# Performance work log

Measured on AMD Instinct MI355X. Metric: run time of the kernel, lower is better.

The kernel has to match this reference:

```python
import jax, jax.numpy as jnp
import numpy as np
import math

NUM_CONVS = 4
GN_GROUPS = 32
GN_EPS = 1e-5
FPN_STRIDES = (8, 16, 32, 64, 128)
PRIOR_PROB = 0.01


def conv3x3(x, w, b):
    # x: [N,C,H,W], w: [O,I,3,3]
    y = jax.lax.conv_general_dilated(
        x, w, window_strides=(1, 1), padding='SAME',
        dimension_numbers=('NCHW', 'OIHW', 'NCHW'))
    return y + b[None, :, None, None]


def group_norm(x, gamma, beta):
    n, c, h, w = x.shape
    xg = x.reshape(n, GN_GROUPS, c // GN_GROUPS, h, w)
    mean = xg.mean(axis=(2, 3, 4), keepdims=True)
    var = xg.var(axis=(2, 3, 4), keepdims=True)
    xn = ((xg - mean) * jax.lax.rsqrt(var + GN_EPS)).reshape(n, c, h, w)
    return xn * gamma[None, :, None, None] + beta[None, :, None, None]


def subnet(x, ws, bs, gws, gbs):
    # NUM_CONVS x (conv3x3 -> GN -> ReLU)
    for i in range(NUM_CONVS):
        x = jax.nn.relu(group_norm(conv3x3(x, ws[i], bs[i]), gws[i], gbs[i]))
    return x


def permute_to_N_HWA_K(x, k):
    n = x.shape[0]
    return x.transpose(0, 2, 3, 1).reshape(n, -1, k)


def setup_inputs() -> dict:
    key = jax.random.key(0)
    ks = jax.random.split(key, 16)
    C, K = 256, 80
    feats = {
        'p3': jax.random.normal(ks[0], (1, C, 80, 80), jnp.float32),
        'p4': jax.random.normal(ks[1], (1, C, 40, 40), jnp.float32),
        'p5': jax.random.normal(ks[2], (1, C, 20, 20), jnp.float32),
        'p6': jax.random.normal(ks[3], (1, C, 10, 10), jnp.float32),
        'p7': jax.random.normal(ks[4], (1, C, 5, 5), jnp.float32),
    }
    std = 0.01
    bias_value = -math.log((1 - PRIOR_PROB) / PRIOR_PROB)
    params = {
        'cls_w': std * jax.random.normal(ks[5], (NUM_CONVS, C, C, 3, 3), jnp.float32),
        'cls_b': jnp.zeros((NUM_CONVS, C), jnp.float32),
        'cls_gn_w': jnp.ones((NUM_CONVS, C), jnp.float32),
        'cls_gn_b': jnp.zeros((NUM_CONVS, C), jnp.float32),
        'box_w': std * jax.random.normal(ks[6], (NUM_CONVS, C, C, 3, 3), jnp.float32),
        'box_b': jnp.zeros((NUM_CONVS, C), jnp.float32),
        'box_gn_w': jnp.ones((NUM_CONVS, C), jnp.float32),
        'box_gn_b': jnp.zeros((NUM_CONVS, C), jnp.float32),
        'score_w': std * jax.random.normal(ks[7], (K, C, 3, 3), jnp.float32),
        'score_b': jnp.full((K,), bias_value, jnp.float32),
        'pred_w': std * jax.random.normal(ks[8], (4, C, 3, 3), jnp.float32),
        'pred_b': jnp.zeros((4,), jnp.float32),
        'iou_w': std * jax.random.normal(ks[9], (1, C, 3, 3), jnp.float32),
        'iou_b': jnp.zeros((1,), jnp.float32),
        'scales': jnp.ones((5,), jnp.float32),
    }
    return {**feats, **params}


def reference(p3, p4, p5, p6, p7,
              cls_w, cls_b, cls_gn_w, cls_gn_b,
              box_w, box_b, box_gn_w, box_gn_b,
              score_w, score_b, pred_w, pred_b, iou_w, iou_b, scales):
    features = [p3, p4, p5, p6, p7]
    logits, bbox_reg, ious = [], [], []
    for l, feat in enumerate(features):
        c = subnet(feat, cls_w, cls_b, cls_gn_w, cls_gn_b)
        b = subnet(feat, box_w, box_b, box_gn_w, box_gn_b)
        logit = conv3x3(c, score_w, score_b)          # [N,80,H,W]
        iou = conv3x3(b, iou_w, iou_b)                # [N,1,H,W]
        bp = conv3x3(b, pred_w, pred_b) * scales[l]   # Scale module
        # norm_reg_targets=True branch
        reg = jax.nn.relu(bp) * FPN_STRIDES[l]        # [N,4,H,W]
        logits.append(permute_to_N_HWA_K(logit, 80))
        bbox_reg.append(permute_to_N_HWA_K(reg, 4))
        ious.append(permute_to_N_HWA_K(iou, 1))
    box_cls = jnp.concatenate(logits, axis=1)    # [N, sumHW, 80]
    box_delta = jnp.concatenate(bbox_reg, axis=1)  # [N, sumHW, 4]
    box_iou = jnp.concatenate(ious, axis=1)      # [N, sumHW, 1]
    # pack into one array for a single output: [N, sumHW, 85]
    return jnp.concatenate([box_cls, box_delta, box_iou], axis=-1)
```

## Files before the change

### kernel.cpp

```cpp
#include <hip/hip_runtime.h>

typedef unsigned short u16;
typedef __attribute__((ext_vector_type(8))) short bf16x8;
typedef __attribute__((ext_vector_type(4))) float f32x4;

#define NLEV 5
#define CCH 256
#define KTOT 2304
#define P_TOT 8525
#define PP_TOT 9165
#define PLS (PP_TOT*64)
#define HSTR 11776

__constant__ int   c_HW[NLEV]     = {6400, 1600, 400, 100, 25};
__constant__ int   c_W[NLEV]      = {80, 40, 20, 10, 5};
__constant__ int   c_off[NLEV]    = {0, 6400, 8000, 8400, 8500};
__constant__ int   c_poff[NLEV]   = {0, 6724, 8488, 8972, 9116};
__constant__ int   c_tls[NLEV+1]  = {0, 50, 65, 71, 73, 74};
__constant__ int   c_ntx[NLEV]    = {5, 3, 2, 1, 1};
__constant__ float c_stridef[NLEV]= {8.f, 16.f, 32.f, 64.f, 128.f};

__device__ __forceinline__ u16 f2bf(float f){
  union { float f; unsigned u; } v; v.f = f;
  unsigned r = v.u + 0x7fffu + ((v.u >> 16) & 1u);
  return (u16)(r >> 16);
}

__device__ __forceinline__ void g2l16(const u16* g, u16* l, int lane){
#if defined(__has_builtin)
#if __has_builtin(__builtin_amdgcn_global_load_lds)
  __builtin_amdgcn_global_load_lds(
      (const __attribute__((address_space(1))) unsigned int*)g,
      (__attribute__((address_space(3))) unsigned int*)l, 16, 0, 0);
  return;
#endif
#endif
  *(uint4*)(l + lane*8) = *(const uint4*)g;
}

#define WAIT_VM12  0x0F7C

template<int MODE>
__global__ __launch_bounds__(128, 2) void gemm_conv(
    const u16* __restrict__ Xc, const u16* __restrict__ Xb,
    const u16* __restrict__ Wc, const u16* __restrict__ Wb,
    const float* __restrict__ bc, const float* __restrict__ bb,
    float* __restrict__ Yc, float* __restrict__ Yb,
    float* __restrict__ stats,
    const float* __restrict__ predb, const float* __restrict__ ioub,
    const float* __restrict__ scales, float* __restrict__ out)
{
  __shared__ u16 hB[2*HSTR];
  __shared__ float sstat[8][2];

  const int ptile = blockIdx.x;
  const int mtile = blockIdx.y;
  const int br = blockIdx.z;
  int lv = 0;
  #pragma unroll
  for (int i = 1; i < NLEV; i++) if (ptile >= c_tls[i]) lv = i;
  const int tidx = ptile - c_tls[lv];
  const int ntx = c_ntx[lv];
  const int ty0 = (tidx / ntx) * 8, tx0 = (tidx - (tidx / ntx) * ntx) * 16;
  const int W = c_W[lv], wrow2 = W + 2;

  const int tid = threadIdx.x, wv = tid >> 6, ln = tid & 63;
  const int quad = ln >> 4, l15 = ln & 15;

  const u16* __restrict__ X  = br ? Xb : Xc;
  const u16* __restrict__ WA = br ? Wb : Wc;

  const int SZ = (MODE == 0) ? 16384 : 8192;
  const int g2 = mtile*2 + wv;
  const u16* aln = WA + (size_t)(g2*2048 + ln*8);

  const u16* hptr[12]; int hslab[12];
  #pragma unroll
  for (int i = 0; i < 12; i++) {
    int j = wv + 2*i;
    if (j > 22) j -= 2;
    hslab[i] = j;
    const int item = j*64 + ln;
    int hp = item >> 3; if (hp >= 180) hp -= 180;
    const int g = item & 7;
    const int hy = hp / 18, hx = hp - hy*18;
    const int prow = c_poff[lv] + (ty0 + hy)*wrow2 + tx0 + hx;
    hptr[i] = X + (size_t)prow*64 + ((g ^ (hp & 7)) << 3);
  }

  auto stageH = [&](int plane) {
    u16* dst = &hB[(plane & 1) * HSTR];
    const size_t cof = (size_t)plane * PLS;
    #pragma unroll
    for (int i = 0; i < 12; i++)
      g2l16(hptr[i] + cof, dst + hslab[i]*512, ln);
  };

  f32x4 acc[2][8];
  #pragma unroll
  for (int i = 0; i < 2; i++)
    #pragma unroll
    for (int j = 0; j < 8; j++) acc[i][j] = (f32x4){0.f, 0.f, 0.f, 0.f};

  bf16x8 af[3][2][2];
  auto loadA = [&](int cc_, int dw_) {
    #pragma unroll
    for (int dh = 0; dh < 3; dh++) {
      const u16* p = aln + (size_t)((dh*3 + dw_)*4 + cc_) * SZ;
      #pragma unroll
      for (int sub = 0; sub < 2; sub++)
        #pragma unroll
        for (int mt = 0; mt < 2; mt++)
          af[dh][sub][mt] = *(const bf16x8*)(p + (sub*2 + mt)*512);
    }
  };

  if (MODE == 0 && tid < 16) sstat[tid >> 1][tid & 1] = 0.f;

  stageH(0);
  stageH(1);
  loadA(0, 0);
  __syncthreads();

  int cc = 0, dw = 0;
  #pragma unroll 1
  for (int u = 0; u < 12; u++) {
    if (dw == 0 && cc > 0) {
      __builtin_amdgcn_s_waitcnt(WAIT_VM12);
      __builtin_amdgcn_sched_barrier(0);
      __builtin_amdgcn_s_barrier();
      __builtin_amdgcn_sched_barrier(0);
      if (cc < 3) stageH(cc + 1);
    }
    const u16* hpl = &hB[(cc & 1) * HSTR];
    #pragma unroll
    for (int sub = 0; sub < 2; sub++) {
      const int q = sub*4 + quad;
      bf16x8 bf[10];
      #pragma unroll
      for (int n2 = 0; n2 < 10; n2++) {
        const int hp = n2*18 + l15 + dw;
        bf[n2] = *(const bf16x8*)&hpl[hp*64 + ((q ^ (hp & 7)) << 3)];
      }
      #pragma unroll
      for (int dh = 0; dh < 3; dh++)
        #pragma unroll
        for (int mt = 0; mt < 2; mt++)
          #pragma unroll
          for (int nt = 0; nt < 8; nt++)
            acc[mt][nt] = __builtin_amdgcn_mfma_f32_16x16x32_bf16(
                af[dh][sub][mt], bf[nt + dh], acc[mt][nt], 0, 0, 0);
    }
    int dwn = dw + 1, ccn = cc;
    if (dwn == 3) { dwn = 0; ccn++; }
    if (u < 11) loadA(ccn, dwn);
    dw = dwn; cc = ccn;
  }

  const int gx = tx0 + l15;
  if (MODE == 0) {
    const float* __restrict__ bias = br ? bb : bc;
    float* __restrict__ Y = br ? Yb : Yc;
    #pragma unroll
    for (int mt = 0; mt < 2; mt++) {
      const int mloc = wv*32 + mt*16 + quad*4;
      const int mrow = mtile*64 + mloc;
      const f32x4 bv = *(const f32x4*)&bias[mrow];
      float s = 0.f, sq = 0.f;
      #pragma unroll
      for (int nt = 0; nt < 8; nt++) {
        const int gy = ty0 + nt;
        f32x4 v = acc[mt][nt] + bv;
        if (gy < W && gx < W) {
          const size_t n = (size_t)(c_off[lv] + gy*W + gx);
          *(f32x4*)&Y[n*CCH + mrow] = v;
          #pragma unroll
          for (int r = 0; r < 4; r++) { s += v[r]; sq += v[r]*v[r]; }
        }
      }
      #pragma unroll
      for (int o = 1; o < 16; o <<= 1) { s += __shfl_xor(s, o); sq += __shfl_xor(sq, o); }
      if (l15 == 0) {
        const int g = mloc >> 3;
        atomicAdd(&sstat[g][0], s);
        atomicAdd(&sstat[g][1], sq);
      }
    }
    __syncthreads();
    if (tid < 16) {
      const int g = tid >> 1, c = tid & 1;
      atomicAdd(&stats[((br*NLEV + lv)*32 + mtile*8 + g)*2 + c], sstat[g][c]);
    }
  } else {
    const float scl = scales[lv];
    const float stf = c_stridef[lv];
    #pragma unroll
    for (int mt = 0; mt < 2; mt++) {
      const int mr0 = mtile*64 + wv*32 + mt*16 + quad*4;
      if (mr0 >= 85) continue;
      #pragma unroll
      for (int nt = 0; nt < 8; nt++) {
        const int gy = ty0 + nt;
        if (gy >= W || gx >= W) continue;
        const size_t n = (size_t)(c_off[lv] + gy*W + gx);
        const f32x4 v = acc[mt][nt];
        #pragma unroll
        for (int r = 0; r < 4; r++) {
          const int m = mr0 + r;
          if (br == 0) {
            if (m < 80) out[n*85 + m] = v[r] + bc[m];
          } else {
            if (m < 4) {
              const float t = (v[r] + predb[m]) * scl;
              out[n*85 + 80 + m] = fmaxf(t, 0.f) * stf;
            } else if (m == 4) {
              out[n*85 + 84] = v[r] + ioub[0];
            }
          }
        }
      }
    }
  }
}

__global__ __launch_bounds__(256) void gn_relu(
    const float* __restrict__ Yc, const float* __restrict__ Yb,
    const float* __restrict__ stats,
    const float* __restrict__ gwc, const float* __restrict__ gbc,
    const float* __restrict__ gwb, const float* __restrict__ gbb,
    u16* __restrict__ Xc, u16* __restrict__ Xb)
{
  const int t = blockIdx.x * 256 + threadIdx.x;
  if (t >= 2 * P_TOT * 32) return;
  const int br = t / (P_TOT * 32);
  const int r  = t - br * (P_TOT * 32);
  const int pg = r >> 5;
  const int c0 = (r & 31) << 3;
  int lv = 0;
  #pragma unroll
  for (int i = 1; i < NLEV; i++) if (pg >= c_off[i]) lv = i;
  const int pl = pg - c_off[lv];
  const int Wl = c_W[lv];
  const int g = c0 >> 3;
  const float* st = &stats[(((size_t)br*NLEV + lv)*32 + g)*2];
  const float cnt = 8.f * (float)c_HW[lv];
  const float mean = st[0] / cnt;
  const float var  = st[1] / cnt - mean*mean;
  const float rstd = rsqrtf(var + 1e-5f);
  const float* Y  = br ? Yb : Yc;
  const float* gw = br ? gwb : gwc;
  const float* gb = br ? gbb : gbc;
  u16* X = br ? Xb : Xc;
  const float* y = &Y[(size_t)pg*CCH + c0];
  const int h = pl / Wl, wi = pl - h*Wl;
  const size_t pidx = (size_t)(c_poff[lv] + (h+1)*(Wl+2) + (wi+1));
  union { u16 u[8]; uint4 v; } pk;
  #pragma unroll
  for (int i = 0; i < 8; i++) {
    const float v = (y[i] - mean)*rstd*gw[c0+i] + gb[c0+i];
    pk.u[i] = f2bf(fmaxf(v, 0.f));
  }
  *(uint4*)&X[(size_t)(c0 >> 6)*PLS + pidx*64 + (c0 & 63)] = pk.v;
}

__global__ __launch_bounds__(256) void feat2bf(
    const float* __restrict__ p3, const float* __restrict__ p4,
    const float* __restrict__ p5, const float* __restrict__ p6,
    const float* __restrict__ p7, u16* __restrict__ X)
{
  const int t = blockIdx.x * 256 + threadIdx.x;
  if (t >= P_TOT * 32) return;
  const int pg = t >> 5, c0 = (t & 31) << 3;
  int lv = 0;
  #pragma unroll
  for (int i = 1; i < NLEV; i++) if (pg >= c_off[i]) lv = i;
  const int pl = pg - c_off[lv];
  const float* src = lv==0 ? p3 : lv==1 ? p4 : lv==2 ? p5 : lv==3 ? p6 : p7;
  const int HW = c_HW[lv], Wl = c_W[lv];
  const int h = pl / Wl, wi = pl - h*Wl;
  const size_t pidx = (size_t)(c_poff[lv] + (h+1)*(Wl+2) + (wi+1));
  union { u16 u[8]; uint4 v; } pk;
  #pragma unroll
  for (int i = 0; i < 8; i++)
    pk.u[i] = f2bf(src[(size_t)(c0+i)*HW + pl]);
  *(uint4*)&X[(size_t)(c0 >> 6)*PLS + pidx*64 + (c0 & 63)] = pk.v;
}

__global__ __launch_bounds__(256) void wconv(
    const float* __restrict__ cw, const float* __restrict__ bw,
    u16* __restrict__ Wc, u16* __restrict__ Wb)
{
  const size_t N = (size_t)4*256*KTOT;
  const size_t t = (size_t)blockIdx.x * 256 + threadIdx.x;
  if (t >= 2*N) return;
  const float* src = (t < N) ? cw : bw;
  u16* dst = (t < N) ? Wc : Wb;
  const size_t i = (t < N) ? t : t - N;
  const size_t lc = i / KTOT;
  const int kk = (int)(i - lc*KTOT);
  const int l = (int)(lc >> 8), co = (int)(lc & 255);
  const int tap = kk >> 8, ci = kk & 255;
  const int s = kk >> 6, kl = kk & 63;
  const size_t d = (size_t)l*589824 + (size_t)s*16384 +
      (size_t)((co >> 5)*2048 + (kl >> 5)*1024 + ((co >> 4) & 1)*512 +
               ((kl >> 3) & 3)*128 + (co & 15)*8 + (kl & 7));
  dst[d] = f2bf(src[(lc*256 + ci)*9 + tap]);
}

__global__ __launch_bounds__(256) void hconv(
    const float* __restrict__ sw, const float* __restrict__ pw,
    const float* __restrict__ iw, u16* __restrict__ Whc, u16* __restrict__ Whb)
{
  const int N = 128 * KTOT;
  const int t = blockIdx.x * 256 + threadIdx.x;
  if (t >= 2*N) return;
  const int i = (t < N) ? t : t - N;
  const int co = i / KTOT, kk = i - co*KTOT;
  const int tap = kk >> 8, ci = kk & 255;
  const int s = kk >> 6, kl = kk & 63;
  const size_t d = (size_t)s*8192 +
      (size_t)((co >> 5)*2048 + (kl >> 5)*1024 + ((co >> 4) & 1)*512 +
               ((kl >> 3) & 3)*128 + (co & 15)*8 + (kl & 7));
  float v = 0.f;
  if (t < N) {
    if (co < 80) v = sw[(co*256 + ci)*9 + tap];
    Whc[d] = f2bf(v);
  } else {
    if (co < 4)       v = pw[(co*256 + ci)*9 + tap];
    else if (co == 4) v = iw[ci*9 + tap];
    Whb[d] = f2bf(v);
  }
}

extern "C" void kernel_launch(void* const* d_in, const int* in_sizes, int n_in,
                              void* d_out, int out_size, void* d_ws, size_t ws_size,
                              hipStream_t stream)
{
  const float* p3      = (const float*)d_in[0];
  const float* p4      = (const float*)d_in[1];
  const float* p5      = (const float*)d_in[2];
  const float* p6      = (const float*)d_in[3];
  const float* p7      = (const float*)d_in[4];
  const float* cls_w   = (const float*)d_in[5];
  const float* cls_b   = (const float*)d_in[6];
  const float* cls_gw  = (const float*)d_in[7];
  const float* cls_gb  = (const float*)d_in[8];
  const float* box_w   = (const float*)d_in[9];
  const float* box_b   = (const float*)d_in[10];
  const float* box_gw  = (const float*)d_in[11];
  const float* box_gb  = (const float*)d_in[12];
  const float* score_w = (const float*)d_in[13];
  const float* score_b = (const float*)d_in[14];
  const float* pred_w  = (const float*)d_in[15];
  const float* pred_b  = (const float*)d_in[16];
  const float* iou_w   = (const float*)d_in[17];
  const float* iou_b   = (const float*)d_in[18];
  const float* scales  = (const float*)d_in[19];
  float* out = (float*)d_out;

  char* w = (char*)d_ws;
  size_t o = 0;
  auto alloc = [&](size_t b) { void* p = w + o; o += (b + 255) & ~(size_t)255; return p; };
  u16*   XF = (u16*)alloc((size_t)PP_TOT*CCH*2);
  u16*   XC = (u16*)alloc((size_t)PP_TOT*CCH*2);
  u16*   XB = (u16*)alloc((size_t)PP_TOT*CCH*2);
  float* ST = (float*)alloc((size_t)4*2*NLEV*32*2*4);
  u16*  WRC = (u16*)alloc((size_t)4*256*KTOT*2);
  u16*  WRB = (u16*)alloc((size_t)4*256*KTOT*2);
  u16*  WHC = (u16*)alloc((size_t)128*KTOT*2);
  u16*  WHB = (u16*)alloc((size_t)128*KTOT*2);
  float* YC = (float*)alloc((size_t)P_TOT*CCH*4);
  float* YB = (float*)alloc((size_t)P_TOT*CCH*4);

  hipMemsetAsync(XF, 0, (size_t)3*PP_TOT*CCH*2 + (size_t)4*2*NLEV*32*2*4, stream);

  wconv<<<dim3((unsigned)(((size_t)2*4*256*KTOT + 255)/256)), 256, 0, stream>>>(cls_w, box_w, WRC, WRB);
  hconv<<<dim3((2*128*KTOT + 255)/256), 256, 0, stream>>>(score_w, pred_w, iou_w, WHC, WHB);
  feat2bf<<<dim3((P_TOT*32 + 255)/256), 256, 0, stream>>>(p3, p4, p5, p6, p7, XF);

  const u16* xci = XF; const u16* xbi = XF;
  for (int l = 0; l < 4; l++) {
    float* STl = ST + (size_t)l*2*NLEV*32*2;
    gemm_conv<0><<<dim3(74, 4, 2), 128, 0, stream>>>(
        xci, xbi, WRC + (size_t)l*589824, WRB + (size_t)l*589824,
        cls_b + l*256, box_b + l*256, YC, YB, STl,
        nullptr, nullptr, nullptr, nullptr);
    gn_relu<<<dim3((2*P_TOT*32 + 255)/256), 256, 0, stream>>>(
        YC, YB, STl, cls_gw + l*256, cls_gb + l*256, box_gw + l*256, box_gb + l*256,
        XC, XB);
    xci = XC; xbi = XB;
  }
  gemm_conv<1><<<dim3(74, 2, 2), 128, 0, stream>>>(
      xci, xbi, WHC, WHB, score_b, nullptr, nullptr, nullptr, nullptr,
      pred_b, iou_b, scales, out);
}
```

Before: 331.0 us.

## Replace LDS-staged halo with direct global register loads in single-wave conv blocks

The conv GEMM kernel no longer stages input halo tiles into shared memory with global_load_lds and barriers. Each block is now a single 64-lane wave that loads B fragments straight from global (L1/L2) into registers, double-buffered across 24 K-stages, over a flattened 1D grid. GN statistics go straight to global atomics instead of through an LDS reduction. This removes LDS traffic and block barriers but reloads overlapping halo data from cache for every stage and raises VGPR pressure.

New measurement: 484.1 us. +46.2%, slower.

```diff
diff --git a/kernel.cpp b/kernel.cpp
--- a/kernel.cpp
+++ b/kernel.cpp
@@ -10,7 +10,6 @@
 #define P_TOT 8525
 #define PP_TOT 9165
 #define PLS (PP_TOT*64)
-#define HSTR 11776
 
 __constant__ int   c_HW[NLEV]     = {6400, 1600, 400, 100, 25};
 __constant__ int   c_W[NLEV]      = {80, 40, 20, 10, 5};
@@ -26,22 +25,10 @@
   return (u16)(r >> 16);
 }
 
-__device__ __forceinline__ void g2l16(const u16* g, u16* l, int lane){
-#if defined(__has_builtin)
-#if __has_builtin(__builtin_amdgcn_global_load_lds)
-  __builtin_amdgcn_global_load_lds(
-      (const __attribute__((address_space(1))) unsigned int*)g,
-      (__attribute__((address_space(3))) unsigned int*)l, 16, 0, 0);
-  return;
-#endif
-#endif
-  *(uint4*)(l + lane*8) = *(const uint4*)g;
-}
-
-#define WAIT_VM12  0x0F7C
-
 template<int MODE>
-__global__ __launch_bounds__(128, 2) void gemm_conv(
+__global__ __launch_bounds__(64)
+__attribute__((amdgpu_waves_per_eu(2, 2)))
+void gemm_conv(
     const u16* __restrict__ Xc, const u16* __restrict__ Xb,
     const u16* __restrict__ Wc, const u16* __restrict__ Wb,
     const float* __restrict__ bc, const float* __restrict__ bb,
@@ -50,12 +37,12 @@
     const float* __restrict__ predb, const float* __restrict__ ioub,
     const float* __restrict__ scales, float* __restrict__ out)
 {
-  __shared__ u16 hB[2*HSTR];
-  __shared__ float sstat[8][2];
-
-  const int ptile = blockIdx.x;
-  const int mtile = blockIdx.y;
-  const int br = blockIdx.z;
+  const int bid = blockIdx.x;
+  const int ptile = bid % 74;
+  const int j     = bid / 74;
+  const int g2 = (MODE == 0) ? (j & 7) : (j < 3 ? j : 0);
+  const int br = (MODE == 0) ? (j >> 3) : (j == 3 ? 1 : 0);
+
   int lv = 0;
   #pragma unroll
   for (int i = 1; i < NLEV; i++) if (ptile >= c_tls[i]) lv = i;
@@ -64,97 +51,58 @@
   const int ty0 = (tidx / ntx) * 8, tx0 = (tidx - (tidx / ntx) * ntx) * 16;
   const int W = c_W[lv], wrow2 = W + 2;
 
-  const int tid = threadIdx.x, wv = tid >> 6, ln = tid & 63;
+  const int ln = threadIdx.x & 63;
   const int quad = ln >> 4, l15 = ln & 15;
 
   const u16* __restrict__ X  = br ? Xb : Xc;
   const u16* __restrict__ WA = br ? Wb : Wc;
 
   const int SZ = (MODE == 0) ? 16384 : 8192;
-  const int g2 = mtile*2 + wv;
   const u16* aln = WA + (size_t)(g2*2048 + ln*8);
-
-  const u16* hptr[12]; int hslab[12];
-  #pragma unroll
-  for (int i = 0; i < 12; i++) {
-    int j = wv + 2*i;
-    if (j > 22) j -= 2;
-    hslab[i] = j;
-    const int item = j*64 + ln;
-    int hp = item >> 3; if (hp >= 180) hp -= 180;
-    const int g = item & 7;
-    const int hy = hp / 18, hx = hp - hy*18;
-    const int prow = c_poff[lv] + (ty0 + hy)*wrow2 + tx0 + hx;
-    hptr[i] = X + (size_t)prow*64 + ((g ^ (hp & 7)) << 3);
-  }
-
-  auto stageH = [&](int plane) {
-    u16* dst = &hB[(plane & 1) * HSTR];
-    const size_t cof = (size_t)plane * PLS;
-    #pragma unroll
-    for (int i = 0; i < 12; i++)
-      g2l16(hptr[i] + cof, dst + hslab[i]*512, ln);
+  const u16* xb0 = X + (size_t)(c_poff[lv] + ty0*wrow2 + tx0 + l15) * 64
+                     + quad*8;
+  const int brow = wrow2 * 64;
+
+  f32x4 acc[2][8];
+  #pragma unroll
+  for (int i = 0; i < 2; i++)
+    #pragma unroll
+    for (int jj = 0; jj < 8; jj++) acc[i][jj] = (f32x4){0.f, 0.f, 0.f, 0.f};
+
+  bf16x8 aA[6], bA[10], aB[6], bB[10];
+
+  auto ldStage = [&](int k, bf16x8 (&a)[6], bf16x8 (&b)[10]) {
+    const int u = k >> 1, s = k & 1;
+    const int cc = u / 3, dw = u - cc*3;
+    #pragma unroll
+    for (int dh = 0; dh < 3; dh++)
+      #pragma unroll
+      for (int mt = 0; mt < 2; mt++)
+        a[dh*2 + mt] = *(const bf16x8*)
+            (aln + (size_t)((dh*3 + dw)*4 + cc) * SZ + (s*2 + mt)*512);
+    const u16* bp = xb0 + (size_t)cc * PLS + (size_t)dw * 64 + s*32;
+    #pragma unroll
+    for (int n2 = 0; n2 < 10; n2++)
+      b[n2] = *(const bf16x8*)(bp + (size_t)n2 * brow);
   };
-
-  f32x4 acc[2][8];
-  #pragma unroll
-  for (int i = 0; i < 2; i++)
-    #pragma unroll
-    for (int j = 0; j < 8; j++) acc[i][j] = (f32x4){0.f, 0.f, 0.f, 0.f};
-
-  bf16x8 af[3][2][2];
-  auto loadA = [&](int cc_, int dw_) {
-    #pragma unroll
-    for (int dh = 0; dh < 3; dh++) {
-      const u16* p = aln + (size_t)((dh*3 + dw_)*4 + cc_) * SZ;
-      #pragma unroll
-      for (int sub = 0; sub < 2; sub++)
+  auto cmpStage = [&](bf16x8 (&a)[6], bf16x8 (&b)[10]) {
+    #pragma unroll
+    for (int dh = 0; dh < 3; dh++)
+      #pragma unroll
+      for (int mt = 0; mt < 2; mt++)
         #pragma unroll
-        for (int mt = 0; mt < 2; mt++)
-          af[dh][sub][mt] = *(const bf16x8*)(p + (sub*2 + mt)*512);
-    }
+        for (int nt = 0; nt < 8; nt++)
+          acc[mt][nt] = __builtin_amdgcn_mfma_f32_16x16x32_bf16(
+              a[dh*2 + mt], b[nt + dh], acc[mt][nt], 0, 0, 0);
   };
 
-  if (MODE == 0 && tid < 16) sstat[tid >> 1][tid & 1] = 0.f;
-
-  stageH(0);
-  stageH(1);
-  loadA(0, 0);
-  __syncthreads();
-
-  int cc = 0, dw = 0;
+  ldStage(0, aA, bA);
   #pragma unroll 1
-  for (int u = 0; u < 12; u++) {
-    if (dw == 0 && cc > 0) {
-      __builtin_amdgcn_s_waitcnt(WAIT_VM12);
-      __builtin_amdgcn_sched_barrier(0);
-      __builtin_amdgcn_s_barrier();
-      __builtin_amdgcn_sched_barrier(0);
-      if (cc < 3) stageH(cc + 1);
-    }
-    const u16* hpl = &hB[(cc & 1) * HSTR];
-    #pragma unroll
-    for (int sub = 0; sub < 2; sub++) {
-      const int q = sub*4 + quad;
-      bf16x8 bf[10];
-      #pragma unroll
-      for (int n2 = 0; n2 < 10; n2++) {
-        const int hp = n2*18 + l15 + dw;
-        bf[n2] = *(const bf16x8*)&hpl[hp*64 + ((q ^ (hp & 7)) << 3)];
-      }
-      #pragma unroll
-      for (int dh = 0; dh < 3; dh++)
-        #pragma unroll
-        for (int mt = 0; mt < 2; mt++)
-          #pragma unroll
-          for (int nt = 0; nt < 8; nt++)
-            acc[mt][nt] = __builtin_amdgcn_mfma_f32_16x16x32_bf16(
-                af[dh][sub][mt], bf[nt + dh], acc[mt][nt], 0, 0, 0);
-    }
-    int dwn = dw + 1, ccn = cc;
-    if (dwn == 3) { dwn = 0; ccn++; }
-    if (u < 11) loadA(ccn, dwn);
-    dw = dwn; cc = ccn;
+  for (int k = 0; k < 24; k += 2) {
+    if (k + 1 < 24) ldStage(k + 1, aB, bB);
+    cmpStage(aA, bA);
+    if (k + 2 < 24) ldStage(k + 2, aA, bA);
+    cmpStage(aB, bB);
   }
 
   const int gx = tx0 + l15;
@@ -163,8 +111,7 @@
     float* __restrict__ Y = br ? Yb : Yc;
     #pragma unroll
     for (int mt = 0; mt < 2; mt++) {
-      const int mloc = wv*32 + mt*16 + quad*4;
-      const int mrow = mtile*64 + mloc;
+      const int mrow = g2*32 + mt*16 + quad*4;
       const f32x4 bv = *(const f32x4*)&bias[mrow];
       float s = 0.f, sq = 0.f;
       #pragma unroll
@@ -181,22 +128,17 @@
       #pragma unroll
       for (int o = 1; o < 16; o <<= 1) { s += __shfl_xor(s, o); sq += __shfl_xor(sq, o); }
       if (l15 == 0) {
-        const int g = mloc >> 3;
-        atomicAdd(&sstat[g][0], s);
-        atomicAdd(&sstat[g][1], sq);
+        const int G = g2*4 + mt*2 + (quad >> 1);
+        atomicAdd(&stats[((br*NLEV + lv)*32 + G)*2 + 0], s);
+        atomicAdd(&stats[((br*NLEV + lv)*32 + G)*2 + 1], sq);
       }
-    }
-    __syncthreads();
-    if (tid < 16) {
-      const int g = tid >> 1, c = tid & 1;
-      atomicAdd(&stats[((br*NLEV + lv)*32 + mtile*8 + g)*2 + c], sstat[g][c]);
     }
   } else {
     const float scl = scales[lv];
     const float stf = c_stridef[lv];
     #pragma unroll
     for (int mt = 0; mt < 2; mt++) {
-      const int mr0 = mtile*64 + wv*32 + mt*16 + quad*4;
+      const int mr0 = g2*32 + mt*16 + quad*4;
       if (mr0 >= 85) continue;
       #pragma unroll
       for (int nt = 0; nt < 8; nt++) {
@@ -381,7 +323,7 @@
   const u16* xci = XF; const u16* xbi = XF;
   for (int l = 0; l < 4; l++) {
     float* STl = ST + (size_t)l*2*NLEV*32*2;
-    gemm_conv<0><<<dim3(74, 4, 2), 128, 0, stream>>>(
+    gemm_conv<0><<<dim3(1184), 64, 0, stream>>>(
         xci, xbi, WRC + (size_t)l*589824, WRB + (size_t)l*589824,
         cls_b + l*256, box_b + l*256, YC, YB, STl,
         nullptr, nullptr, nullptr, nullptr);
@@ -390,7 +332,7 @@
         XC, XB);
     xci = XC; xbi = XB;
   }
-  gemm_conv<1><<<dim3(74, 2, 2), 128, 0, stream>>>(
+  gemm_conv<1><<<dim3(296), 64, 0, stream>>>(
       xci, xbi, WHC, WHB, score_b, nullptr, nullptr, nullptr, nullptr,
       pred_b, iou_b, scales, out);
 }
```
